# Performance work log

Hardware: AMD Instinct MI355X
Metric: run time of the kernel (lower is better)

The kernel has to match this reference:

```python
import jax, jax.numpy as jnp
import numpy as np

B, L, D_MODEL, N_HEAD, D_K, D_V, VOCAB = 2, 1024, 512, 8, 64, 64, 64
TEMP = float(np.sqrt(D_K))
LN_EPS = 1e-5


def setup_inputs() -> dict:
    key = jax.random.key(0)
    ks = jax.random.split(key, 24)
    inp = {}
    inp['q'] = jax.random.normal(ks[0], (B, L, D_MODEL), jnp.float32)
    inp['k'] = jax.random.normal(ks[1], (B, L, D_MODEL), jnp.float32)
    inp['v'] = jax.random.normal(ks[2], (B, L, D_MODEL), jnp.float32)
    inp['mask'] = jax.random.uniform(ks[3], (B, L, L)) < 0.1
    # tf_f1 carries -1 (padding) positions; its sign defines tf_mask for ALL five features
    inp['tf_f1'] = jax.random.randint(ks[4], (B, L, L), -1, VOCAB, jnp.int32)
    inp['tf_f2'] = jax.random.randint(ks[5], (B, L, L), 0, VOCAB, jnp.int32)
    inp['tf_f3'] = jax.random.randint(ks[6], (B, L, L), 0, VOCAB, jnp.int32)
    inp['tf_f4'] = jax.random.randint(ks[7], (B, L, L), 0, VOCAB, jnp.int32)
    inp['tf_f5'] = jax.random.randint(ks[8], (B, L, L), 0, VOCAB, jnp.int32)
    s_qk = np.sqrt(2.0 / (D_MODEL + D_K))
    s_v = np.sqrt(2.0 / (D_MODEL + D_V))
    inp['w_q'] = jax.random.normal(ks[9], (D_MODEL, N_HEAD * D_K), jnp.float32) * s_qk
    inp['b_q'] = jnp.zeros((N_HEAD * D_K,), jnp.float32)
    inp['w_k'] = jax.random.normal(ks[10], (D_MODEL, N_HEAD * D_K), jnp.float32) * s_qk
    inp['b_k'] = jnp.zeros((N_HEAD * D_K,), jnp.float32)
    inp['w_v'] = jax.random.normal(ks[11], (D_MODEL, N_HEAD * D_V), jnp.float32) * s_v
    inp['b_v'] = jnp.zeros((N_HEAD * D_V,), jnp.float32)
    for i in range(5):
        inp[f'emb{i+1}'] = jax.random.normal(ks[12 + i], (VOCAB, N_HEAD), jnp.float32)
    fc_std = np.sqrt(2.0 / (N_HEAD * D_V + D_MODEL))
    inp['fc_w'] = jax.random.normal(ks[17], (N_HEAD * D_V, D_MODEL), jnp.float32) * fc_std
    inp['fc_b'] = jnp.zeros((D_MODEL,), jnp.float32)
    inp['ln_g'] = jnp.ones((D_MODEL,), jnp.float32)
    inp['ln_b'] = jnp.zeros((D_MODEL,), jnp.float32)
    return inp


def _bias(emb, tf, tf_mask):
    # (tf * mask).long() embedding lookup, zeroed where mask==0 -> [H, B, L, L]
    idx = (tf.astype(jnp.float32) * tf_mask).astype(jnp.int32)
    feat = emb[idx] * tf_mask[..., None]          # [B, L, L, H]
    return jnp.transpose(feat, (3, 0, 1, 2))      # [H, B, L, L]


def reference(q, k, v, mask, tf_f1, tf_f2, tf_f3, tf_f4, tf_f5,
              w_q, b_q, w_k, b_k, w_v, b_v,
              emb1, emb2, emb3, emb4, emb5,
              fc_w, fc_b, ln_g, ln_b):
    residual = q
    qh = (q @ w_q + b_q).reshape(B, L, N_HEAD, D_K)
    kh = (k @ w_k + b_k).reshape(B, L, N_HEAD, D_K)
    vh = (v @ w_v + b_v).reshape(B, L, N_HEAD, D_V)

    scores = jnp.einsum('blhd,bmhd->hblm', qh, kh)  # [H, B, Lq, Lk]
    tf_mask = (tf_f1 >= 0).astype(jnp.float32)      # [B, L, L] (from tf_f1 only, as in torch)
    scores = (scores
              + _bias(emb1, tf_f1, tf_mask)
              + _bias(emb2, tf_f2, tf_mask)
              + _bias(emb3, tf_f3, tf_mask)
              + _bias(emb4, tf_f4, tf_mask)
              + _bias(emb5, tf_f5, tf_mask)) / TEMP
    scores = jnp.where(mask[None], -jnp.inf, scores)
    attn = jax.nn.softmax(scores, axis=-1)          # [H, B, L, L]; dropout = identity (eval)

    out = jnp.einsum('hblm,bmhd->blhd', attn, vh).reshape(B, L, N_HEAD * D_V)
    out = out @ fc_w + fc_b                          # dropout = identity (eval)
    out = out + residual
    mu = jnp.mean(out, axis=-1, keepdims=True)
    var = jnp.mean((out - mu) ** 2, axis=-1, keepdims=True)
    out = (out - mu) * jax.lax.rsqrt(var + LN_EPS) * ln_g + ln_b
    return out, attn.reshape(N_HEAD * B, L, L)
```

## Files before the change

kernel.cpp:

```cpp
#include <hip/hip_runtime.h>
#include <math.h>

#define L_SEQ 1024
#define DMODEL 512
#define NHEAD 8
#define NB 2

typedef __attribute__((ext_vector_type(8))) short bf8;
typedef __attribute__((ext_vector_type(4))) float f4;

__device__ __forceinline__ short f2bf(float f) {
    unsigned u = __float_as_uint(f);
    unsigned r = u + 0x7FFF + ((u >> 16) & 1);
    return (short)(r >> 16);
}

__global__ __launch_bounds__(256) void cast_bf16_kernel(
    const float* __restrict__ src, short* __restrict__ dst, int n4)
{
    int i = blockIdx.x * 256 + threadIdx.x;
    if (i < n4) {
        float4 f = ((const float4*)src)[i];
        short4 o;
        o.x = f2bf(f.x); o.y = f2bf(f.y); o.z = f2bf(f.z); o.w = f2bf(f.w);
        ((short4*)dst)[i] = o;
    }
}

__global__ __launch_bounds__(256) void transpose_cast_kernel(
    const float* __restrict__ s0, const float* __restrict__ s1,
    const float* __restrict__ s2, const float* __restrict__ s3,
    short* __restrict__ d0, short* __restrict__ d1,
    short* __restrict__ d2, short* __restrict__ d3)
{
    const float* src; short* dst;
    switch (blockIdx.z) {
        case 0: src = s0; dst = d0; break;
        case 1: src = s1; dst = d1; break;
        case 2: src = s2; dst = d2; break;
        default: src = s3; dst = d3; break;
    }
    __shared__ float tile[32][33];
    const int tx = threadIdx.x, ty = threadIdx.y;
    const int x0 = blockIdx.x * 32, y0 = blockIdx.y * 32;
#pragma unroll
    for (int j = 0; j < 32; j += 8)
        tile[ty + j][tx] = src[(size_t)(y0 + ty + j) * 512 + x0 + tx];
    __syncthreads();
#pragma unroll
    for (int j = 0; j < 32; j += 8)
        dst[(size_t)(x0 + ty + j) * 512 + y0 + tx] = f2bf(tile[tx][ty + j]);
}

template<int MODE>
__global__ __launch_bounds__(256) void gemm_mfma_kernel(
    const short* __restrict__ A, const short* __restrict__ Bt,
    const float* __restrict__ bias, void* __restrict__ Cout)
{
    const int w = threadIdx.x >> 6, lane = threadIdx.x & 63;
    const int lr = lane & 15, lq = lane >> 4;
    const int m_base = blockIdx.y * 64 + w * 16;
    const int n_base = blockIdx.x * 64;

    f4 acc[4];
    const f4 zero = {0.f, 0.f, 0.f, 0.f};
#pragma unroll
    for (int nf = 0; nf < 4; ++nf) acc[nf] = zero;

    for (int k0 = 0; k0 < 512; k0 += 32) {
        bf8 a = *(const bf8*)(A + (size_t)(m_base + lr) * 512 + k0 + lq * 8);
#pragma unroll
        for (int nf = 0; nf < 4; ++nf) {
            bf8 b = *(const bf8*)(Bt + (size_t)(n_base + nf * 16 + lr) * 512 + k0 + lq * 8);
            acc[nf] = __builtin_amdgcn_mfma_f32_16x16x32_bf16(a, b, acc[nf], 0, 0, 0);
        }
    }

#pragma unroll
    for (int nf = 0; nf < 4; ++nf) {
        const int n = n_base + nf * 16 + lr;
        const float bv = bias[n];
        const int mrow = m_base + lq * 4;
#pragma unroll
        for (int r = 0; r < 4; ++r) {
            const float val = acc[nf][r] + bv;
            const int m = mrow + r;
            if (MODE == 0) {
                ((short*)Cout)[(size_t)m * 512 + n] = f2bf(val);
            } else if (MODE == 1) {
                const int bb = m >> 10, l = m & 1023;
                ((short*)Cout)[((size_t)bb * 512 + n) * 1024 + l] = f2bf(val);
            } else {
                ((float*)Cout)[(size_t)m * 512 + n] = val;
            }
        }
    }
}

__global__ __launch_bounds__(256) void scores_mfma_kernel(
    const short* __restrict__ qh, const short* __restrict__ kh,
    float* __restrict__ sc)
{
    const int z = blockIdx.z, h = z >> 1, b = z & 1;
    const int w = threadIdx.x >> 6, lane = threadIdx.x & 63;
    const int wr = w >> 1, wc = w & 1;
    const int lr = lane & 15, lq = lane >> 4;
    const int l0 = blockIdx.y * 128 + wr * 64;
    const int m0 = blockIdx.x * 128 + wc * 64;
    const int colb = h * 64 + lq * 8;
    const size_t base = (size_t)b * L_SEQ * DMODEL;

    bf8 afr[4][2], bfr[4][2];
#pragma unroll
    for (int i = 0; i < 4; ++i)
#pragma unroll
        for (int kk = 0; kk < 2; ++kk) {
            afr[i][kk] = *(const bf8*)(qh + base + (size_t)(l0 + i * 16 + lr) * 512 + colb + kk * 32);
            bfr[i][kk] = *(const bf8*)(kh + base + (size_t)(m0 + i * 16 + lr) * 512 + colb + kk * 32);
        }

    f4 acc[4][4];
    const f4 zero = {0.f, 0.f, 0.f, 0.f};
#pragma unroll
    for (int mt = 0; mt < 4; ++mt)
#pragma unroll
        for (int nt = 0; nt < 4; ++nt) acc[mt][nt] = zero;

#pragma unroll
    for (int kk = 0; kk < 2; ++kk)
#pragma unroll
        for (int mt = 0; mt < 4; ++mt)
#pragma unroll
            for (int nt = 0; nt < 4; ++nt)
                acc[mt][nt] = __builtin_amdgcn_mfma_f32_16x16x32_bf16(
                    afr[mt][kk], bfr[nt][kk], acc[mt][nt], 0, 0, 0);

    float* out = sc + (size_t)z * L_SEQ * L_SEQ;
#pragma unroll
    for (int mt = 0; mt < 4; ++mt)
#pragma unroll
        for (int nt = 0; nt < 4; ++nt)
#pragma unroll
            for (int r = 0; r < 4; ++r)
                out[(size_t)(l0 + mt * 16 + lq * 4 + r) * 1024 + m0 + nt * 16 + lr] = acc[mt][nt][r];
}

__global__ __launch_bounds__(256) void bias_softmax_kernel(
    float* __restrict__ attn,
    const int* __restrict__ mask,
    const int* __restrict__ tf1, const int* __restrict__ tf2,
    const int* __restrict__ tf3, const int* __restrict__ tf4,
    const int* __restrict__ tf5,
    const float* __restrict__ emb1, const float* __restrict__ emb2,
    const float* __restrict__ emb3, const float* __restrict__ emb4,
    const float* __restrict__ emb5)
{
    const int l = blockIdx.x, b = blockIdx.y, t = threadIdx.x;
    __shared__ float embs[5][NHEAD][64];
    __shared__ float s[NHEAD][L_SEQ];
    __shared__ float rinv[NHEAD];

    {
        const float* es[5] = {emb1, emb2, emb3, emb4, emb5};
        for (int i = t; i < 5 * 512; i += 256) {
            int j = i >> 9, rem = i & 511;
            int h = rem >> 6, idx = rem & 63;
            embs[j][h][idx] = es[j][idx * NHEAD + h];
        }
    }
    __syncthreads();

    const size_t rowbase = ((size_t)(b * L_SEQ + l)) * L_SEQ;
#pragma unroll
    for (int c = 0; c < 4; ++c) {
        const int m = (c << 8) + t;
        const int am  = mask[rowbase + m];
        const int t1v = tf1[rowbase + m];
        float bias8[NHEAD];
        if (t1v >= 0) {
            const int i2 = tf2[rowbase + m];
            const int i3 = tf3[rowbase + m];
            const int i4 = tf4[rowbase + m];
            const int i5 = tf5[rowbase + m];
#pragma unroll
            for (int h = 0; h < NHEAD; ++h)
                bias8[h] = embs[0][h][t1v] + embs[1][h][i2] + embs[2][h][i3]
                         + embs[3][h][i4] + embs[4][h][i5];
        } else {
#pragma unroll
            for (int h = 0; h < NHEAD; ++h) bias8[h] = 0.f;
        }
#pragma unroll
        for (int h = 0; h < NHEAD; ++h) {
            const float raw = attn[(((size_t)(h * NB + b)) * L_SEQ + l) * L_SEQ + m];
            s[h][m] = am ? -INFINITY : (raw + bias8[h]) * 0.125f;
        }
    }
    __syncthreads();

    {
        const int h = t >> 5, i = t & 31;
        float mx = -INFINITY;
        for (int m = i; m < L_SEQ; m += 32) mx = fmaxf(mx, s[h][m]);
#pragma unroll
        for (int off = 16; off; off >>= 1) mx = fmaxf(mx, __shfl_down(mx, off, 32));
        mx = __shfl(mx, 0, 32);
        float sm = 0.f;
        for (int m = i; m < L_SEQ; m += 32) {
            float e = __expf(s[h][m] - mx);
            s[h][m] = e;
            sm += e;
        }
#pragma unroll
        for (int off = 16; off; off >>= 1) sm += __shfl_down(sm, off, 32);
        if (i == 0) rinv[h] = 1.0f / sm;
    }
    __syncthreads();

    float inv[NHEAD];
#pragma unroll
    for (int h = 0; h < NHEAD; ++h) inv[h] = rinv[h];
    for (int m = t; m < L_SEQ; m += 256) {
#pragma unroll
        for (int h = 0; h < NHEAD; ++h)
            attn[(((size_t)(h * NB + b)) * L_SEQ + l) * L_SEQ + m] = s[h][m] * inv[h];
    }
}

__global__ __launch_bounds__(256) void av_mfma_kernel(
    const float* __restrict__ attn, const short* __restrict__ vht,
    short* __restrict__ pv)
{
    const int z = blockIdx.y, h = z >> 1, b = z & 1;
    const int w = threadIdx.x >> 6, lane = threadIdx.x & 63;
    const int lr = lane & 15, lq = lane >> 4;
    const int l0 = blockIdx.x * 128 + w * 32;
    const float* Ab = attn + (size_t)z * L_SEQ * L_SEQ;
    const short* Bb = vht + ((size_t)b * 512 + h * 64) * 1024;

    f4 acc[2][4];
    const f4 zero = {0.f, 0.f, 0.f, 0.f};
#pragma unroll
    for (int mt = 0; mt < 2; ++mt)
#pragma unroll
        for (int nt = 0; nt < 4; ++nt) acc[mt][nt] = zero;

    for (int k0 = 0; k0 < L_SEQ; k0 += 32) {
        bf8 a[2];
#pragma unroll
        for (int mt = 0; mt < 2; ++mt) {
            const float* p = Ab + (size_t)(l0 + mt * 16 + lr) * 1024 + k0 + lq * 8;
            float4 f0 = *(const float4*)p;
            float4 f1 = *(const float4*)(p + 4);
            bf8 tv;
            tv[0] = f2bf(f0.x); tv[1] = f2bf(f0.y); tv[2] = f2bf(f0.z); tv[3] = f2bf(f0.w);
            tv[4] = f2bf(f1.x); tv[5] = f2bf(f1.y); tv[6] = f2bf(f1.z); tv[7] = f2bf(f1.w);
            a[mt] = tv;
        }
#pragma unroll
        for (int nt = 0; nt < 4; ++nt) {
            bf8 bv = *(const bf8*)(Bb + (size_t)(nt * 16 + lr) * 1024 + k0 + lq * 8);
            acc[0][nt] = __builtin_amdgcn_mfma_f32_16x16x32_bf16(a[0], bv, acc[0][nt], 0, 0, 0);
            acc[1][nt] = __builtin_amdgcn_mfma_f32_16x16x32_bf16(a[1], bv, acc[1][nt], 0, 0, 0);
        }
    }

#pragma unroll
    for (int nt = 0; nt < 4; ++nt) {
        const int n = nt * 16 + lr;
#pragma unroll
        for (int mt = 0; mt < 2; ++mt) {
            const int rowb = l0 + mt * 16 + lq * 4;
#pragma unroll
            for (int r = 0; r < 4; ++r)
                pv[(size_t)(b * L_SEQ + rowb + r) * 512 + h * 64 + n] = f2bf(acc[mt][nt][r]);
        }
    }
}

__global__ __launch_bounds__(256) void ln_kernel(
    const float* __restrict__ x, const float* __restrict__ res,
    const float* __restrict__ g, const float* __restrict__ bvec,
    float* __restrict__ out)
{
    const int row = blockIdx.x;
    const int t = threadIdx.x;
    float2 xv = ((const float2*)(x + (size_t)row * DMODEL))[t];
    float2 rv = ((const float2*)(res + (size_t)row * DMODEL))[t];
    const float a = xv.x + rv.x;
    const float c = xv.y + rv.y;
    float s = a + c, sq = a * a + c * c;
#pragma unroll
    for (int off = 32; off; off >>= 1) {
        s  += __shfl_down(s, off);
        sq += __shfl_down(sq, off);
    }
    __shared__ float ssum[4], ssq[4];
    __shared__ float smu, srs;
    const int wid = t >> 6, lane = t & 63;
    if (lane == 0) { ssum[wid] = s; ssq[wid] = sq; }
    __syncthreads();
    if (t == 0) {
        float ts = ssum[0] + ssum[1] + ssum[2] + ssum[3];
        float tq = ssq[0] + ssq[1] + ssq[2] + ssq[3];
        float mu = ts * (1.0f / DMODEL);
        float var = tq * (1.0f / DMODEL) - mu * mu;
        smu = mu;
        srs = rsqrtf(var + 1e-5f);
    }
    __syncthreads();
    const float mu = smu, rs = srs;
    float2 gv = ((const float2*)g)[t];
    float2 bv = ((const float2*)bvec)[t];
    float2 o;
    o.x = (a - mu) * rs * gv.x + bv.x;
    o.y = (c - mu) * rs * gv.y + bv.y;
    ((float2*)(out + (size_t)row * DMODEL))[t] = o;
}

extern "C" void kernel_launch(void* const* d_in, const int* in_sizes, int n_in,
                              void* d_out, int out_size, void* d_ws, size_t ws_size,
                              hipStream_t stream)
{
    const float* q    = (const float*)d_in[0];
    const float* k    = (const float*)d_in[1];
    const float* v    = (const float*)d_in[2];
    const int*   mask = (const int*)d_in[3];
    const int*   tf1  = (const int*)d_in[4];
    const int*   tf2  = (const int*)d_in[5];
    const int*   tf3  = (const int*)d_in[6];
    const int*   tf4  = (const int*)d_in[7];
    const int*   tf5  = (const int*)d_in[8];
    const float* w_q  = (const float*)d_in[9];
    const float* b_q  = (const float*)d_in[10];
    const float* w_k  = (const float*)d_in[11];
    const float* b_k  = (const float*)d_in[12];
    const float* w_v  = (const float*)d_in[13];
    const float* b_v  = (const float*)d_in[14];
    const float* emb1 = (const float*)d_in[15];
    const float* emb2 = (const float*)d_in[16];
    const float* emb3 = (const float*)d_in[17];
    const float* emb4 = (const float*)d_in[18];
    const float* emb5 = (const float*)d_in[19];
    const float* fc_w = (const float*)d_in[20];
    const float* fc_b = (const float*)d_in[21];
    const float* ln_g = (const float*)d_in[22];
    const float* ln_b = (const float*)d_in[23];

    float* out  = (float*)d_out;
    float* attn = out + (size_t)NB * L_SEQ * DMODEL;

    char* wsb = (char*)d_ws;
    short* qb   = (short*)(wsb + 0);
    short* kb   = (short*)(wsb + (2u << 20));
    short* vb   = (short*)(wsb + (4u << 20));
    short* Wtq  = (short*)(wsb + (6u << 20));
    short* Wtk  = (short*)(wsb + (6u << 20) + (512u << 10));
    short* Wtv  = (short*)(wsb + (7u << 20));
    short* Wtfc = (short*)(wsb + (7u << 20) + (512u << 10));
    short* qh   = (short*)(wsb + (8u << 20));
    short* kh   = (short*)(wsb + (10u << 20));
    short* vht  = (short*)(wsb + (12u << 20));
    short* pv   = (short*)(wsb + (14u << 20));
    float* fco  = (float*)(wsb + (16u << 20));

    const int n4 = NB * L_SEQ * DMODEL / 4;

    cast_bf16_kernel<<<n4 / 256, 256, 0, stream>>>(q, qb, n4);
    cast_bf16_kernel<<<n4 / 256, 256, 0, stream>>>(k, kb, n4);
    cast_bf16_kernel<<<n4 / 256, 256, 0, stream>>>(v, vb, n4);

    transpose_cast_kernel<<<dim3(16, 16, 4), dim3(32, 8), 0, stream>>>(
        w_q, w_k, w_v, fc_w, Wtq, Wtk, Wtv, Wtfc);

    dim3 gproj(DMODEL / 64, NB * L_SEQ / 64);
    gemm_mfma_kernel<0><<<gproj, 256, 0, stream>>>(qb, Wtq, b_q, qh);
    gemm_mfma_kernel<0><<<gproj, 256, 0, stream>>>(kb, Wtk, b_k, kh);
    gemm_mfma_kernel<1><<<gproj, 256, 0, stream>>>(vb, Wtv, b_v, vht);

    scores_mfma_kernel<<<dim3(8, 8, 16), 256, 0, stream>>>(qh, kh, attn);

    bias_softmax_kernel<<<dim3(L_SEQ, NB), 256, 0, stream>>>(
        attn, mask, tf1, tf2, tf3, tf4, tf5, emb1, emb2, emb3, emb4, emb5);

    av_mfma_kernel<<<dim3(8, 16), 256, 0, stream>>>(attn, vht, pv);

    gemm_mfma_kernel<2><<<gproj, 256, 0, stream>>>(pv, Wtfc, fc_b, fco);

    ln_kernel<<<NB * L_SEQ, 256, 0, stream>>>(fco, q, ln_g, ln_b, out);
}
```

Baseline: 334.7 us.

## Keep bias-softmax rows in registers with vectorized loads and wave-shuffle reductions

Rewrites the bias+softmax kernel so each thread owns four contiguous columns for all eight heads. Mask, feature and score data are read with 16-byte vector loads, and the rows stay in registers instead of a 32KB shared-memory staging buffer. Max and sum are reduced with 64-wide xor shuffles plus a small cross-wave shared reduction. Freeing the shared memory and adding a launch-bounds occupancy hint should let more blocks reside per CU, at the cost of higher register pressure and always doing the embedding lookups, including for padded positions.

```diff
diff --git a/kernel.cpp b/kernel.cpp
--- a/kernel.cpp
+++ b/kernel.cpp
@@ -145,7 +145,7 @@
                 out[(size_t)(l0 + mt * 16 + lq * 4 + r) * 1024 + m0 + nt * 16 + lr] = acc[mt][nt][r];
 }
 
-__global__ __launch_bounds__(256) void bias_softmax_kernel(
+__global__ __launch_bounds__(256, 4) void bias_softmax_kernel(
     float* __restrict__ attn,
     const int* __restrict__ mask,
     const int* __restrict__ tf1, const int* __restrict__ tf2,
@@ -157,73 +157,106 @@
 {
     const int l = blockIdx.x, b = blockIdx.y, t = threadIdx.x;
     __shared__ float embs[5][NHEAD][64];
-    __shared__ float s[NHEAD][L_SEQ];
-    __shared__ float rinv[NHEAD];
+    __shared__ float redmx[4][NHEAD];
+    __shared__ float redsm[4][NHEAD];
 
     {
         const float* es[5] = {emb1, emb2, emb3, emb4, emb5};
-        for (int i = t; i < 5 * 512; i += 256) {
-            int j = i >> 9, rem = i & 511;
-            int h = rem >> 6, idx = rem & 63;
+#pragma unroll
+        for (int it = 0; it < 10; ++it) {
+            const int i = it * 256 + t;
+            const int j = it >> 1;
+            const int rem = i & 511;
+            const int h = rem >> 6, idx = rem & 63;
             embs[j][h][idx] = es[j][idx * NHEAD + h];
         }
     }
     __syncthreads();
 
-    const size_t rowbase = ((size_t)(b * L_SEQ + l)) * L_SEQ;
-#pragma unroll
-    for (int c = 0; c < 4; ++c) {
-        const int m = (c << 8) + t;
-        const int am  = mask[rowbase + m];
-        const int t1v = tf1[rowbase + m];
-        float bias8[NHEAD];
-        if (t1v >= 0) {
-            const int i2 = tf2[rowbase + m];
-            const int i3 = tf3[rowbase + m];
-            const int i4 = tf4[rowbase + m];
-            const int i5 = tf5[rowbase + m];
-#pragma unroll
-            for (int h = 0; h < NHEAD; ++h)
-                bias8[h] = embs[0][h][t1v] + embs[1][h][i2] + embs[2][h][i3]
-                         + embs[3][h][i4] + embs[4][h][i5];
-        } else {
-#pragma unroll
-            for (int h = 0; h < NHEAD; ++h) bias8[h] = 0.f;
-        }
-#pragma unroll
-        for (int h = 0; h < NHEAD; ++h) {
-            const float raw = attn[(((size_t)(h * NB + b)) * L_SEQ + l) * L_SEQ + m];
-            s[h][m] = am ? -INFINITY : (raw + bias8[h]) * 0.125f;
-        }
-    }
-    __syncthreads();
-
-    {
-        const int h = t >> 5, i = t & 31;
-        float mx = -INFINITY;
-        for (int m = i; m < L_SEQ; m += 32) mx = fmaxf(mx, s[h][m]);
-#pragma unroll
-        for (int off = 16; off; off >>= 1) mx = fmaxf(mx, __shfl_down(mx, off, 32));
-        mx = __shfl(mx, 0, 32);
-        float sm = 0.f;
-        for (int m = i; m < L_SEQ; m += 32) {
-            float e = __expf(s[h][m] - mx);
-            s[h][m] = e;
-            sm += e;
-        }
-#pragma unroll
-        for (int off = 16; off; off >>= 1) sm += __shfl_down(sm, off, 32);
-        if (i == 0) rinv[h] = 1.0f / sm;
-    }
-    __syncthreads();
-
-    float inv[NHEAD];
-#pragma unroll
-    for (int h = 0; h < NHEAD; ++h) inv[h] = rinv[h];
-    for (int m = t; m < L_SEQ; m += 256) {
-#pragma unroll
-        for (int h = 0; h < NHEAD; ++h)
-            attn[(((size_t)(h * NB + b)) * L_SEQ + l) * L_SEQ + m] = s[h][m] * inv[h];
+    const size_t rowbase = ((size_t)(b * L_SEQ + l)) * L_SEQ + (size_t)(t * 4);
+    const int4 mk  = *(const int4*)(mask + rowbase);
+    const int4 i1v = *(const int4*)(tf1 + rowbase);
+    const int4 i2v = *(const int4*)(tf2 + rowbase);
+    const int4 i3v = *(const int4*)(tf3 + rowbase);
+    const int4 i4v = *(const int4*)(tf4 + rowbase);
+    const int4 i5v = *(const int4*)(tf5 + rowbase);
+
+    f4 av[NHEAD];
+#pragma unroll
+    for (int h = 0; h < NHEAD; ++h)
+        av[h] = *(const f4*)(attn + ((size_t)(h * NB + b) * L_SEQ + l) * L_SEQ + t * 4);
+
+#define BIAS_FOLD(MI, I1, I2, I3, I4, I5, MK)                                   \
+    {                                                                           \
+        const float tfm = ((I1) >= 0) ? 1.0f : 0.0f;                            \
+        const int c1 = ((I1) >= 0) ? (I1) : 0;                                  \
+        _Pragma("unroll")                                                       \
+        for (int h = 0; h < NHEAD; ++h) {                                       \
+            const float bsum = embs[0][h][c1] + embs[1][h][I2]                  \
+                             + embs[2][h][I3] + embs[3][h][I4]                  \
+                             + embs[4][h][I5];                                  \
+            av[h][MI] = (MK) ? -INFINITY                                        \
+                             : (av[h][MI] + bsum * tfm) * 0.125f;               \
+        }                                                                       \
+    }
+
+    BIAS_FOLD(0, i1v.x, i2v.x, i3v.x, i4v.x, i5v.x, mk.x)
+    BIAS_FOLD(1, i1v.y, i2v.y, i3v.y, i4v.y, i5v.y, mk.y)
+    BIAS_FOLD(2, i1v.z, i2v.z, i3v.z, i4v.z, i5v.z, mk.z)
+    BIAS_FOLD(3, i1v.w, i2v.w, i3v.w, i4v.w, i5v.w, mk.w)
+#undef BIAS_FOLD
+
+    const int wid = t >> 6, lane = t & 63;
+
+    float mx[NHEAD];
+#pragma unroll
+    for (int h = 0; h < NHEAD; ++h)
+        mx[h] = fmaxf(fmaxf(av[h][0], av[h][1]), fmaxf(av[h][2], av[h][3]));
+#pragma unroll
+    for (int h = 0; h < NHEAD; ++h) {
+#pragma unroll
+        for (int off = 1; off < 64; off <<= 1)
+            mx[h] = fmaxf(mx[h], __shfl_xor(mx[h], off));
+    }
+    if (lane == 0) {
+#pragma unroll
+        for (int h = 0; h < NHEAD; ++h) redmx[wid][h] = mx[h];
+    }
+    __syncthreads();
+#pragma unroll
+    for (int h = 0; h < NHEAD; ++h)
+        mx[h] = fmaxf(fmaxf(redmx[0][h], redmx[1][h]),
+                      fmaxf(redmx[2][h], redmx[3][h]));
+
+    float sm[NHEAD];
+#pragma unroll
+    for (int h = 0; h < NHEAD; ++h) {
+        f4 e;
+        e[0] = __expf(av[h][0] - mx[h]);
+        e[1] = __expf(av[h][1] - mx[h]);
+        e[2] = __expf(av[h][2] - mx[h]);
+        e[3] = __expf(av[h][3] - mx[h]);
+        av[h] = e;
+        sm[h] = (e[0] + e[1]) + (e[2] + e[3]);
+    }
+#pragma unroll
+    for (int h = 0; h < NHEAD; ++h) {
+#pragma unroll
+        for (int off = 1; off < 64; off <<= 1)
+            sm[h] += __shfl_xor(sm[h], off);
+    }
+    if (lane == 0) {
+#pragma unroll
+        for (int h = 0; h < NHEAD; ++h) redsm[wid][h] = sm[h];
+    }
+    __syncthreads();
+
+#pragma unroll
+    for (int h = 0; h < NHEAD; ++h) {
+        const float tot = (redsm[0][h] + redsm[1][h]) + (redsm[2][h] + redsm[3][h]);
+        const float inv = 1.0f / tot;
+        f4 o = av[h] * inv;
+        *(f4*)(attn + ((size_t)(h * NB + b) * L_SEQ + l) * L_SEQ + t * 4) = o;
     }
 }
 
```

Measured after the change: 284.7 us. -14.9%, faster.
